# Kernel tuning notes

Hardware: AMD Instinct MI355X
Metric: run time of the kernel (lower is better)

## Reference

```python
import jax, jax.numpy as jnp
import numpy as np

H, W, C, E = 6, 40, 512, 128  # hardcoded in module


def setup_inputs() -> dict:
    key = jax.random.key(0)
    ks = jax.random.split(key, 9)
    nB = 512
    inp = {
        "prev_hidden": jax.random.normal(ks[0], (nB, C), jnp.float32),
        "conv_feats": jax.random.normal(ks[1], (nB, C, H, W), jnp.float32),
        "conv_feats_origin": jax.random.normal(ks[2], (nB, C, H, W), jnp.float32),
        "cur_embeddings": jax.random.normal(ks[3], (nB, E), jnp.float32),
        # params
        "score_w": jax.random.normal(ks[4], (C,), jnp.float32) * (1.0 / np.sqrt(C)),
        "w_ih": jax.random.normal(ks[5], (3 * C, C + E), jnp.float32) * (1.0 / np.sqrt(C)),
        "w_hh": jax.random.normal(ks[6], (3 * C, C), jnp.float32) * (1.0 / np.sqrt(C)),
        "b_ih": jax.random.normal(ks[7], (3 * C,), jnp.float32) * 0.01,
        "b_hh": jax.random.normal(ks[8], (3 * C,), jnp.float32) * 0.01,
    }
    return inp


def gru_cell(x, h, w_ih, w_hh, b_ih, b_hh):
    # PyTorch GRUCell semantics
    gi = x @ w_ih.T + b_ih            # [B, 3C]
    gh = h @ w_hh.T + b_hh            # [B, 3C]
    i_r, i_z, i_n = jnp.split(gi, 3, axis=1)
    h_r, h_z, h_n = jnp.split(gh, 3, axis=1)
    r = jax.nn.sigmoid(i_r + h_r)
    z = jax.nn.sigmoid(i_z + h_z)
    n = jnp.tanh(i_n + r * h_n)
    return (1.0 - z) * n + z * h


def reference(prev_hidden, conv_feats, conv_feats_origin, cur_embeddings,
              score_w, w_ih, w_hh, b_ih, b_hh):
    nB = prev_hidden.shape[0]
    cf = conv_feats.reshape(nB, C, H * W)          # [B, C, HW]
    cfo = conv_feats_origin.reshape(nB, C, H * W)  # [B, C, HW]
    # additive attention score: tanh(feat + h) . score_w
    e = jnp.tanh(cf + prev_hidden[:, :, None])      # [B, C, HW]
    emition = jnp.einsum('bch,c->bh', e, score_w)   # [B, HW]
    alpha = jax.nn.softmax(emition, axis=1)         # softmax over HW positions
    context = jnp.einsum('bch,bh->bc', cfo, alpha)  # [B, C]
    x = jnp.concatenate([context, cur_embeddings], axis=1)  # [B, C+E]
    cur_hidden = gru_cell(x, prev_hidden, w_ih, w_hh, b_ih, b_hh)
    return cur_hidden, alpha.T  # alpha returned as [HW, B] like the original
```

## Files before the change

### kernel.cpp

```cpp
#include <hip/hip_runtime.h>
#include <hip/hip_bf16.h>

#define B   512
#define C   512
#define HW  240
#define E   128
#define XD  640
#define G3  1536

typedef short  s8v  __attribute__((ext_vector_type(8)));
typedef float  f4v  __attribute__((ext_vector_type(4)));

__device__ __forceinline__ float fast_tanh(float x) {
    float ex = __expf(2.0f * x);
    return (ex - 1.0f) * __builtin_amdgcn_rcpf(ex + 1.0f);
}
__device__ __forceinline__ float fast_sigmoid(float x) {
    return __builtin_amdgcn_rcpf(1.0f + __expf(-x));
}
__device__ __forceinline__ unsigned short f2bf(float x) {
    return __builtin_bit_cast(unsigned short, __float2bfloat16(x));
}

__global__ __launch_bounds__(512) void attn_kernel(
    const float* __restrict__ prev_hidden,
    const float* __restrict__ conv_feats,
    const float* __restrict__ conv_feats_origin,
    const float* __restrict__ cur_emb,
    const float* __restrict__ score_w,
    float* __restrict__ alpha_out,
    unsigned short* __restrict__ x_bf16)
{
    const int b = blockIdx.x;
    const int t = threadIdx.x;
    const int lane = t & 63;
    const int w = t >> 6;

    __shared__ float sw_s[C];
    __shared__ float ph_s[C];
    __shared__ float tmp[512];
    __shared__ float af[HW];
    __shared__ float red[8];

    for (int i = t; i < C; i += 512) {
        sw_s[i] = score_w[i];
        ph_s[i] = prev_hidden[b * C + i];
    }
    __syncthreads();

    float acc = 0.f;
    if (t < 480) {
        const int h = t % HW;
        const int c0 = (t / HW) * 256;
        const float* cf = conv_feats + (size_t)b * C * HW + h;
        #pragma unroll 8
        for (int c = 0; c < 256; ++c) {
            float v = cf[(size_t)(c0 + c) * HW];
            acc += fast_tanh(v + ph_s[c0 + c]) * sw_s[c0 + c];
        }
    }
    tmp[t] = acc;
    __syncthreads();

    float e = -1e30f;
    if (t < HW) e = tmp[t] + tmp[t + HW];

    float m = e;
    #pragma unroll
    for (int off = 32; off >= 1; off >>= 1) m = fmaxf(m, __shfl_xor(m, off));
    if (lane == 0) red[w] = m;
    __syncthreads();
    m = red[0];
    #pragma unroll
    for (int i = 1; i < 8; ++i) m = fmaxf(m, red[i]);

    float p = (t < HW) ? __expf(e - m) : 0.f;
    float s = p;
    #pragma unroll
    for (int off = 32; off >= 1; off >>= 1) s += __shfl_xor(s, off);
    __syncthreads();
    if (lane == 0) red[w] = s;
    __syncthreads();
    s = red[0];
    #pragma unroll
    for (int i = 1; i < 8; ++i) s += red[i];
    float inv = __builtin_amdgcn_rcpf(s);

    if (t < HW) {
        float a = p * inv;
        af[t] = a;
        alpha_out[t * B + b] = a;
    }
    __syncthreads();

    {
        const float4* row = (const float4*)(conv_feats_origin +
                                            (size_t)b * C * HW + (size_t)t * HW);
        float ctx = 0.f;
        #pragma unroll 4
        for (int h4 = 0; h4 < HW / 4; ++h4) {
            float4 v = row[h4];
            ctx += v.x * af[4 * h4]     + v.y * af[4 * h4 + 1]
                 + v.z * af[4 * h4 + 2] + v.w * af[4 * h4 + 3];
        }
        x_bf16[(size_t)b * XD + t] = f2bf(ctx);
    }
    if (t < E) x_bf16[(size_t)b * XD + C + t] = f2bf(cur_emb[b * E + t]);
}

__global__ void cvt4_kernel(const float4* __restrict__ src,
                            ushort4* __restrict__ dst, int n4)
{
    int i = blockIdx.x * blockDim.x + threadIdx.x;
    if (i < n4) {
        float4 v = src[i];
        ushort4 o;
        o.x = f2bf(v.x); o.y = f2bf(v.y); o.z = f2bf(v.z); o.w = f2bf(v.w);
        dst[i] = o;
    }
}

__global__ __launch_bounds__(256) void gemm_kernel(
    const unsigned short* __restrict__ x,
    const unsigned short* __restrict__ hprev,
    const unsigned short* __restrict__ wih,
    const unsigned short* __restrict__ whh,
    const float* __restrict__ b_ih, const float* __restrict__ b_hh,
    float* __restrict__ gi, float* __restrict__ gh)
{
    const int z = blockIdx.z;
    const unsigned short* Amat = z ? hprev : x;
    const unsigned short* Wmat = z ? whh : wih;
    const float* bias = z ? b_hh : b_ih;
    float* out = z ? gh : gi;
    const int K = z ? C : XD;

    const int b0 = blockIdx.x * 64;
    const int j0 = blockIdx.y * 64;

    __shared__ alignas(16) unsigned short As[64][40];
    __shared__ alignas(16) unsigned short Ws[64][40];

    const int t = threadIdx.x, lane = t & 63, w = t >> 6;
    const int wm = w & 1, wn = w >> 1;
    const int r = t >> 2, kq = t & 3;
    const int q = lane >> 4, mm = lane & 15;

    f4v z4 = {0.f, 0.f, 0.f, 0.f};
    f4v acc[2][2] = {{z4, z4}, {z4, z4}};

    for (int k0 = 0; k0 < K; k0 += 32) {
        *(s8v*)&As[r][kq * 8] =
            *(const s8v*)&Amat[(size_t)(b0 + r) * K + k0 + kq * 8];
        *(s8v*)&Ws[r][kq * 8] =
            *(const s8v*)&Wmat[(size_t)(j0 + r) * K + k0 + kq * 8];
        __syncthreads();

        s8v a0 = *(const s8v*)&As[wm * 32 + mm][q * 8];
        s8v a1 = *(const s8v*)&As[wm * 32 + 16 + mm][q * 8];
        s8v w0 = *(const s8v*)&Ws[wn * 32 + mm][q * 8];
        s8v w1 = *(const s8v*)&Ws[wn * 32 + 16 + mm][q * 8];

        acc[0][0] = __builtin_amdgcn_mfma_f32_16x16x32_bf16(a0, w0, acc[0][0], 0, 0, 0);
        acc[0][1] = __builtin_amdgcn_mfma_f32_16x16x32_bf16(a0, w1, acc[0][1], 0, 0, 0);
        acc[1][0] = __builtin_amdgcn_mfma_f32_16x16x32_bf16(a1, w0, acc[1][0], 0, 0, 0);
        acc[1][1] = __builtin_amdgcn_mfma_f32_16x16x32_bf16(a1, w1, acc[1][1], 0, 0, 0);
        __syncthreads();
    }

    #pragma unroll
    for (int mi = 0; mi < 2; ++mi)
        #pragma unroll
        for (int ni = 0; ni < 2; ++ni) {
            int jj = j0 + wn * 32 + ni * 16 + mm;
            float bv = bias[jj];
            #pragma unroll
            for (int rg = 0; rg < 4; ++rg) {
                int bi = b0 + wm * 32 + mi * 16 + q * 4 + rg;
                out[(size_t)bi * G3 + jj] = acc[mi][ni][rg] + bv;
            }
        }
}

__global__ void gates_kernel(const float* __restrict__ gi,
                             const float* __restrict__ gh,
                             const float* __restrict__ hprev,
                             float* __restrict__ out)
{
    int idx = blockIdx.x * blockDim.x + threadIdx.x;
    if (idx >= B * C) return;
    int b = idx >> 9;
    int c = idx & 511;
    const float* gib = gi + (size_t)b * G3;
    const float* ghb = gh + (size_t)b * G3;
    float r  = fast_sigmoid(gib[c] + ghb[c]);
    float zz = fast_sigmoid(gib[c + C] + ghb[c + C]);
    float n  = fast_tanh(gib[c + 2 * C] + r * ghb[c + 2 * C]);
    out[idx] = (1.f - zz) * n + zz * hprev[idx];
}

extern "C" void kernel_launch(void* const* d_in, const int* in_sizes, int n_in,
                              void* d_out, int out_size, void* d_ws, size_t ws_size,
                              hipStream_t stream)
{
    const float* prev_hidden = (const float*)d_in[0];
    const float* conv_feats  = (const float*)d_in[1];
    const float* cfo         = (const float*)d_in[2];
    const float* emb         = (const float*)d_in[3];
    const float* score_w     = (const float*)d_in[4];
    const float* w_ih        = (const float*)d_in[5];
    const float* w_hh        = (const float*)d_in[6];
    const float* b_ih        = (const float*)d_in[7];
    const float* b_hh        = (const float*)d_in[8];

    float* out       = (float*)d_out;
    float* alpha_out = out + B * C;

    char* ws = (char*)d_ws;
    unsigned short* x_bf16 = (unsigned short*)(ws);
    unsigned short* h_bf16 = (unsigned short*)(ws + 655360);
    unsigned short* wih_bf = (unsigned short*)(ws + 1179648);
    unsigned short* whh_bf = (unsigned short*)(ws + 3145728);
    float* gi = (float*)(ws + 4718592);
    float* gh = (float*)(ws + 7864320);

    {
        int n4 = (G3 * XD) / 4;
        cvt4_kernel<<<(n4 + 255) / 256, 256, 0, stream>>>((const float4*)w_ih, (ushort4*)wih_bf, n4);
        n4 = (G3 * C) / 4;
        cvt4_kernel<<<(n4 + 255) / 256, 256, 0, stream>>>((const float4*)w_hh, (ushort4*)whh_bf, n4);
        n4 = (B * C) / 4;
        cvt4_kernel<<<(n4 + 255) / 256, 256, 0, stream>>>((const float4*)prev_hidden, (ushort4*)h_bf16, n4);
    }

    attn_kernel<<<B, 512, 0, stream>>>(prev_hidden, conv_feats, cfo, emb, score_w,
                                       alpha_out, x_bf16);

    gemm_kernel<<<dim3(8, 24, 2), 256, 0, stream>>>(x_bf16, h_bf16, wih_bf, whh_bf,
                                                    b_ih, b_hh, gi, gh);

    gates_kernel<<<(B * C + 255) / 256, 256, 0, stream>>>(gi, gh, prev_hidden, out);
}
```

Before: 539.1 us.

## Split attention into emition, softmax and context kernels over channel chunks

The single per-batch attention kernel becomes three kernels. The emition kernel computes partial scores over 64-channel chunks with float4 loads across an 8x larger grid. A small softmax kernel reduces the partials, and a context kernel computes the weighted sum with 4 lanes per row. This raises parallelism and memory-level concurrency on the bandwidth-bound feature reads, at the cost of extra launches and a round trip of partials and alpha through global memory. The three bf16 conversion kernels are merged into one, and the GEMM K-tile is doubled to 64 with loads issued before the barrier.

```diff
diff --git a/kernel.cpp b/kernel.cpp
--- a/kernel.cpp
+++ b/kernel.cpp
@@ -8,6 +8,10 @@
 #define XD  640
 #define G3  1536
 
+#define N4_WIH 245760
+#define N4_WHH 196608
+#define N4_H    65536
+
 typedef short  s8v  __attribute__((ext_vector_type(8)));
 typedef float  f4v  __attribute__((ext_vector_type(4)));
 
@@ -22,57 +26,82 @@
     return __builtin_bit_cast(unsigned short, __float2bfloat16(x));
 }
 
-__global__ __launch_bounds__(512) void attn_kernel(
+__global__ __launch_bounds__(256) void emition_kernel(
     const float* __restrict__ prev_hidden,
     const float* __restrict__ conv_feats,
-    const float* __restrict__ conv_feats_origin,
+    const float* __restrict__ score_w,
+    float* __restrict__ partials)
+{
+    const int b = blockIdx.x;
+    const int chunk = blockIdx.y;
+    const int c0 = chunk * 64;
+    const int t = threadIdx.x;
+
+    __shared__ float ph_s[64], sw_s[64];
+    __shared__ float4 red[4 * 60];
+
+    if (t < 64) {
+        ph_s[t] = prev_hidden[b * C + c0 + t];
+        sw_s[t] = score_w[c0 + t];
+    }
+    __syncthreads();
+
+    if (t < 240) {
+        const int cs = t / 60;
+        const int i  = t % 60;
+        const float4* base =
+            (const float4*)(conv_feats + ((size_t)(b * C + c0 + cs * 16)) * HW) + i;
+        float4 acc = {0.f, 0.f, 0.f, 0.f};
+        #pragma unroll
+        for (int j = 0; j < 16; ++j) {
+            float4 v = base[j * (HW / 4)];
+            float ph = ph_s[cs * 16 + j];
+            float sw = sw_s[cs * 16 + j];
+            acc.x += fast_tanh(v.x + ph) * sw;
+            acc.y += fast_tanh(v.y + ph) * sw;
+            acc.z += fast_tanh(v.z + ph) * sw;
+            acc.w += fast_tanh(v.w + ph) * sw;
+        }
+        red[cs * 60 + i] = acc;
+    }
+    __syncthreads();
+
+    if (t < 60) {
+        float4 a = red[t], b4 = red[60 + t], c4 = red[120 + t], d4 = red[180 + t];
+        float4 s;
+        s.x = a.x + b4.x + c4.x + d4.x;
+        s.y = a.y + b4.y + c4.y + d4.y;
+        s.z = a.z + b4.z + c4.z + d4.z;
+        s.w = a.w + b4.w + c4.w + d4.w;
+        ((float4*)(partials + ((size_t)b * 8 + chunk) * HW))[t] = s;
+    }
+}
+
+__global__ __launch_bounds__(256) void softmax_kernel(
+    const float* __restrict__ partials,
     const float* __restrict__ cur_emb,
-    const float* __restrict__ score_w,
+    float* __restrict__ alpha_f32,
     float* __restrict__ alpha_out,
     unsigned short* __restrict__ x_bf16)
 {
-    const int b = blockIdx.x;
-    const int t = threadIdx.x;
-    const int lane = t & 63;
-    const int w = t >> 6;
-
-    __shared__ float sw_s[C];
-    __shared__ float ph_s[C];
-    __shared__ float tmp[512];
-    __shared__ float af[HW];
-    __shared__ float red[8];
-
-    for (int i = t; i < C; i += 512) {
-        sw_s[i] = score_w[i];
-        ph_s[i] = prev_hidden[b * C + i];
-    }
-    __syncthreads();
-
-    float acc = 0.f;
-    if (t < 480) {
-        const int h = t % HW;
-        const int c0 = (t / HW) * 256;
-        const float* cf = conv_feats + (size_t)b * C * HW + h;
-        #pragma unroll 8
-        for (int c = 0; c < 256; ++c) {
-            float v = cf[(size_t)(c0 + c) * HW];
-            acc += fast_tanh(v + ph_s[c0 + c]) * sw_s[c0 + c];
-        }
-    }
-    tmp[t] = acc;
-    __syncthreads();
+    const int b = blockIdx.x, t = threadIdx.x;
+    const int lane = t & 63, w = t >> 6;
+    __shared__ float red[4];
 
     float e = -1e30f;
-    if (t < HW) e = tmp[t] + tmp[t + HW];
-
+    if (t < HW) {
+        const float* p = partials + (size_t)b * 8 * HW + t;
+        float s0 = 0.f;
+        #pragma unroll
+        for (int k = 0; k < 8; ++k) s0 += p[k * HW];
+        e = s0;
+    }
     float m = e;
     #pragma unroll
     for (int off = 32; off >= 1; off >>= 1) m = fmaxf(m, __shfl_xor(m, off));
     if (lane == 0) red[w] = m;
     __syncthreads();
-    m = red[0];
-    #pragma unroll
-    for (int i = 1; i < 8; ++i) m = fmaxf(m, red[i]);
+    m = fmaxf(fmaxf(red[0], red[1]), fmaxf(red[2], red[3]));
 
     float p = (t < HW) ? __expf(e - m) : 0.f;
     float s = p;
@@ -81,43 +110,61 @@
     __syncthreads();
     if (lane == 0) red[w] = s;
     __syncthreads();
-    s = red[0];
-    #pragma unroll
-    for (int i = 1; i < 8; ++i) s += red[i];
+    s = red[0] + red[1] + red[2] + red[3];
     float inv = __builtin_amdgcn_rcpf(s);
 
     if (t < HW) {
         float a = p * inv;
-        af[t] = a;
-        alpha_out[t * B + b] = a;
-    }
-    __syncthreads();
-
-    {
-        const float4* row = (const float4*)(conv_feats_origin +
-                                            (size_t)b * C * HW + (size_t)t * HW);
-        float ctx = 0.f;
-        #pragma unroll 4
-        for (int h4 = 0; h4 < HW / 4; ++h4) {
-            float4 v = row[h4];
-            ctx += v.x * af[4 * h4]     + v.y * af[4 * h4 + 1]
-                 + v.z * af[4 * h4 + 2] + v.w * af[4 * h4 + 3];
-        }
-        x_bf16[(size_t)b * XD + t] = f2bf(ctx);
+        alpha_f32[b * HW + t] = a;
+        alpha_out[(size_t)t * B + b] = a;
     }
     if (t < E) x_bf16[(size_t)b * XD + C + t] = f2bf(cur_emb[b * E + t]);
 }
 
-__global__ void cvt4_kernel(const float4* __restrict__ src,
-                            ushort4* __restrict__ dst, int n4)
+__global__ __launch_bounds__(256) void context_kernel(
+    const float* __restrict__ cfo,
+    const float* __restrict__ alpha_f32,
+    unsigned short* __restrict__ x_bf16)
+{
+    const int b = blockIdx.x, chunk = blockIdx.y, t = threadIdx.x;
+    const int lane = t & 63, w = t >> 6;
+    __shared__ float4 af4[60];
+    if (t < 60) af4[t] = ((const float4*)(alpha_f32 + b * HW))[t];
+    __syncthreads();
+
+    const int r = chunk * 64 + w * 16 + (lane >> 2);
+    const int q = lane & 3;
+    const float4* row = (const float4*)(cfo + ((size_t)(b * C + r)) * HW);
+
+    float acc = 0.f;
+    #pragma unroll
+    for (int k = 0; k < 15; ++k) {
+        float4 v = row[q + 4 * k];
+        float4 a = af4[q + 4 * k];
+        acc += v.x * a.x + v.y * a.y + v.z * a.z + v.w * a.w;
+    }
+    acc += __shfl_xor(acc, 1);
+    acc += __shfl_xor(acc, 2);
+    if (q == 0) x_bf16[(size_t)b * XD + r] = f2bf(acc);
+}
+
+__global__ void cvt_all_kernel(const float4* __restrict__ wih,
+                               const float4* __restrict__ whh,
+                               const float4* __restrict__ h,
+                               ushort4* __restrict__ wih_o,
+                               ushort4* __restrict__ whh_o,
+                               ushort4* __restrict__ h_o)
 {
     int i = blockIdx.x * blockDim.x + threadIdx.x;
-    if (i < n4) {
-        float4 v = src[i];
-        ushort4 o;
-        o.x = f2bf(v.x); o.y = f2bf(v.y); o.z = f2bf(v.z); o.w = f2bf(v.w);
-        dst[i] = o;
-    }
+    const float4* src; ushort4* dst; int j;
+    if (i < N4_WIH)                { src = wih; dst = wih_o; j = i; }
+    else if (i < N4_WIH + N4_WHH)  { src = whh; dst = whh_o; j = i - N4_WIH; }
+    else if (i < N4_WIH + N4_WHH + N4_H) { src = h; dst = h_o; j = i - N4_WIH - N4_WHH; }
+    else return;
+    float4 v = src[j];
+    ushort4 o;
+    o.x = f2bf(v.x); o.y = f2bf(v.y); o.z = f2bf(v.z); o.w = f2bf(v.w);
+    dst[j] = o;
 }
 
 __global__ __launch_bounds__(256) void gemm_kernel(
@@ -138,8 +185,8 @@
     const int b0 = blockIdx.x * 64;
     const int j0 = blockIdx.y * 64;
 
-    __shared__ alignas(16) unsigned short As[64][40];
-    __shared__ alignas(16) unsigned short Ws[64][40];
+    __shared__ alignas(16) unsigned short As[64][72];
+    __shared__ alignas(16) unsigned short Ws[64][72];
 
     const int t = threadIdx.x, lane = t & 63, w = t >> 6;
     const int wm = w & 1, wn = w >> 1;
@@ -149,23 +196,31 @@
     f4v z4 = {0.f, 0.f, 0.f, 0.f};
     f4v acc[2][2] = {{z4, z4}, {z4, z4}};
 
-    for (int k0 = 0; k0 < K; k0 += 32) {
-        *(s8v*)&As[r][kq * 8] =
-            *(const s8v*)&Amat[(size_t)(b0 + r) * K + k0 + kq * 8];
-        *(s8v*)&Ws[r][kq * 8] =
-            *(const s8v*)&Wmat[(size_t)(j0 + r) * K + k0 + kq * 8];
+    for (int k0 = 0; k0 < K; k0 += 64) {
+        const unsigned short* ga = &Amat[(size_t)(b0 + r) * K + k0 + kq * 8];
+        const unsigned short* gw = &Wmat[(size_t)(j0 + r) * K + k0 + kq * 8];
+        s8v a_lo = *(const s8v*)ga;
+        s8v a_hi = *(const s8v*)(ga + 32);
+        s8v w_lo = *(const s8v*)gw;
+        s8v w_hi = *(const s8v*)(gw + 32);
         __syncthreads();
-
-        s8v a0 = *(const s8v*)&As[wm * 32 + mm][q * 8];
-        s8v a1 = *(const s8v*)&As[wm * 32 + 16 + mm][q * 8];
-        s8v w0 = *(const s8v*)&Ws[wn * 32 + mm][q * 8];
-        s8v w1 = *(const s8v*)&Ws[wn * 32 + 16 + mm][q * 8];
-
-        acc[0][0] = __builtin_amdgcn_mfma_f32_16x16x32_bf16(a0, w0, acc[0][0], 0, 0, 0);
-        acc[0][1] = __builtin_amdgcn_mfma_f32_16x16x32_bf16(a0, w1, acc[0][1], 0, 0, 0);
-        acc[1][0] = __builtin_amdgcn_mfma_f32_16x16x32_bf16(a1, w0, acc[1][0], 0, 0, 0);
-        acc[1][1] = __builtin_amdgcn_mfma_f32_16x16x32_bf16(a1, w1, acc[1][1], 0, 0, 0);
+        *(s8v*)&As[r][kq * 8]      = a_lo;
+        *(s8v*)&As[r][kq * 8 + 32] = a_hi;
+        *(s8v*)&Ws[r][kq * 8]      = w_lo;
+        *(s8v*)&Ws[r][kq * 8 + 32] = w_hi;
         __syncthreads();
+
+        #pragma unroll
+        for (int kk = 0; kk < 2; ++kk) {
+            s8v a0 = *(const s8v*)&As[wm * 32 + mm][kk * 32 + q * 8];
+            s8v a1 = *(const s8v*)&As[wm * 32 + 16 + mm][kk * 32 + q * 8];
+            s8v w0 = *(const s8v*)&Ws[wn * 32 + mm][kk * 32 + q * 8];
+            s8v w1 = *(const s8v*)&Ws[wn * 32 + 16 + mm][kk * 32 + q * 8];
+            acc[0][0] = __builtin_amdgcn_mfma_f32_16x16x32_bf16(a0, w0, acc[0][0], 0, 0, 0);
+            acc[0][1] = __builtin_amdgcn_mfma_f32_16x16x32_bf16(a0, w1, acc[0][1], 0, 0, 0);
+            acc[1][0] = __builtin_amdgcn_mfma_f32_16x16x32_bf16(a1, w0, acc[1][0], 0, 0, 0);
+            acc[1][1] = __builtin_amdgcn_mfma_f32_16x16x32_bf16(a1, w1, acc[1][1], 0, 0, 0);
+        }
     }
 
     #pragma unroll
@@ -217,24 +272,25 @@
     float* alpha_out = out + B * C;
 
     char* ws = (char*)d_ws;
-    unsigned short* x_bf16 = (unsigned short*)(ws);
-    unsigned short* h_bf16 = (unsigned short*)(ws + 655360);
-    unsigned short* wih_bf = (unsigned short*)(ws + 1179648);
-    unsigned short* whh_bf = (unsigned short*)(ws + 3145728);
-    float* gi = (float*)(ws + 4718592);
-    float* gh = (float*)(ws + 7864320);
+    float* partials          = (float*)(ws);
+    float* gi                = (float*)(ws);
+    float* gh                = (float*)(ws + 3932160);
+    float* alpha_f32         = (float*)(ws + 7077888);
+    unsigned short* x_bf16   = (unsigned short*)(ws + 7569408);
+    unsigned short* h_bf16   = (unsigned short*)(ws + 8224768);
+    unsigned short* wih_bf   = (unsigned short*)(ws + 8749056);
+    unsigned short* whh_bf   = (unsigned short*)(ws + 10715136);
 
     {
-        int n4 = (G3 * XD) / 4;
-        cvt4_kernel<<<(n4 + 255) / 256, 256, 0, stream>>>((const float4*)w_ih, (ushort4*)wih_bf, n4);
-        n4 = (G3 * C) / 4;
-        cvt4_kernel<<<(n4 + 255) / 256, 256, 0, stream>>>((const float4*)w_hh, (ushort4*)whh_bf, n4);
-        n4 = (B * C) / 4;
-        cvt4_kernel<<<(n4 + 255) / 256, 256, 0, stream>>>((const float4*)prev_hidden, (ushort4*)h_bf16, n4);
-    }
-
-    attn_kernel<<<B, 512, 0, stream>>>(prev_hidden, conv_feats, cfo, emb, score_w,
-                                       alpha_out, x_bf16);
+        int n4 = N4_WIH + N4_WHH + N4_H;
+        cvt_all_kernel<<<(n4 + 255) / 256, 256, 0, stream>>>(
+            (const float4*)w_ih, (const float4*)w_hh, (const float4*)prev_hidden,
+            (ushort4*)wih_bf, (ushort4*)whh_bf, (ushort4*)h_bf16);
+    }
+
+    emition_kernel<<<dim3(B, 8), 256, 0, stream>>>(prev_hidden, conv_feats, score_w, partials);
+    softmax_kernel<<<B, 256, 0, stream>>>(partials, emb, alpha_f32, alpha_out, x_bf16);
+    context_kernel<<<dim3(B, 8), 256, 0, stream>>>(cfo, alpha_f32, x_bf16);
 
     gemm_kernel<<<dim3(8, 24, 2), 256, 0, stream>>>(x_bf16, h_bf16, wih_bf, whh_bf,
                                                     b_ih, b_hh, gi, gh);
```

Measured after the change: 520.6 us. -3.4%, faster.
